# Kernel optimization log

Hardware: AMD Instinct MI355X
Metric: run time of the kernel (lower is better)

## Reference

```python
import jax, jax.numpy as jnp
import numpy as np

N, E, G, H, D = 30000, 480000, 128, 4, 64
NF, EF, GF, L = 92, 50, 108, 5
EPS = 1e-3  # keras BatchNormalization default epsilon


def _bn(t, g, b, m, v):
    # inference-mode batch norm with running stats
    return (t - m) * jax.lax.rsqrt(v + EPS) * g + b


def _forward(x, edge_attr, global_features,
             node_W, node_b, edge_W, edge_b,
             conv_W, conv_att, conv_bias, conv_bn_g, conv_bn_b, conv_bn_m, conv_bn_v,
             ga_W0, ga_b0, ga_bn0_g, ga_bn0_b, ga_bn0_m, ga_bn0_v,
             ga_W1, ga_b1, ga_bn1_g, ga_bn1_b, ga_bn1_m, ga_bn1_v,
             ga_W2, ga_b2, out_W0, out_b0, out_W1, out_b1,
             edge_index, batch_idx, num_graphs):
    lrelu = lambda t: jax.nn.leaky_relu(t, 0.2)
    row, col = edge_index[0], edge_index[1]
    n = x.shape[0]

    x = lrelu(x @ node_W + node_b)          # [N, D] node embedding
    ea = lrelu(edge_attr @ edge_W + edge_b)  # [E, D] edge embedding

    def conv(xc, p):
        W, att, bias, g, b, m, v = p
        xi = (jnp.concatenate([xc[row], ea], -1) @ W).reshape(-1, H, D)  # [E,H,D]
        xj = (jnp.concatenate([xc[col], ea], -1) @ W).reshape(-1, H, D)
        score = jnp.einsum('ehd,hd->eh', jnp.concatenate([xi, xj], -1), att)
        a = jnp.exp(_bn(lrelu(score), g, b, m, v))            # [E,H]
        norm = jax.ops.segment_sum(a, row, num_segments=n)    # edge softmax denom
        a = a / norm[row]
        msg = xj * a[..., None]                               # [E,H,D]
        # faithful to original: transpose then flat reshape before scatter-add
        msg = jnp.transpose(msg, (1, 0, 2)).reshape(-1, H * D)
        agg = jax.ops.segment_sum(msg, row, num_segments=n)
        out = agg.reshape(n, H, D).mean(axis=1) + bias
        return xc + out, None  # residual connection (done in GATGNN.call)

    x, _ = jax.lax.scan(conv, x, (conv_W, conv_att, conv_bias,
                                  conv_bn_g, conv_bn_b, conv_bn_m, conv_bn_v))

    # global attention pooling
    feat = jnp.concatenate([x, global_features[batch_idx]], -1)  # [N, D+GF]
    h = jax.nn.relu(_bn(feat @ ga_W0 + ga_b0, ga_bn0_g, ga_bn0_b, ga_bn0_m, ga_bn0_v))
    h = jax.nn.relu(_bn(h @ ga_W1 + ga_b1, ga_bn1_g, ga_bn1_b, ga_bn1_m, ga_bn1_v))
    a = jnp.exp(h @ ga_W2 + ga_b2)                               # [N,1]
    norm = jax.ops.segment_sum(a, batch_idx, num_segments=num_graphs)
    a = a / norm[batch_idx]
    pooled = jax.ops.segment_sum(x * a, batch_idx, num_segments=num_graphs)  # [G,D]
    out = jax.nn.relu(pooled @ out_W0 + out_b0) @ out_W1 + out_b1
    return out.squeeze(-1)  # output_dim == 1


def setup_inputs() -> dict:
    key = jax.random.key(0)
    ks = jax.random.split(key, 16)
    s = 0.05
    return {
        'x': jax.random.normal(ks[0], (N, NF), jnp.float32),
        'edge_attr': jax.random.normal(ks[1], (E, EF), jnp.float32),
        'global_features': jax.random.normal(ks[2], (G, GF), jnp.float32),
        'node_W': jax.random.normal(ks[3], (NF, D)) * s, 'node_b': jnp.zeros((D,)),
        'edge_W': jax.random.normal(ks[4], (EF, D)) * s, 'edge_b': jnp.zeros((D,)),
        'conv_W': jax.random.normal(ks[5], (L, 2 * D, H * D)) * s,
        'conv_att': jax.random.normal(ks[6], (L, H, 2 * D)) * s,
        'conv_bias': jnp.zeros((L, D)),
        'conv_bn_g': jnp.ones((L, H)), 'conv_bn_b': jnp.zeros((L, H)),
        'conv_bn_m': jnp.zeros((L, H)), 'conv_bn_v': jnp.ones((L, H)),
        'ga_W0': jax.random.normal(ks[7], (D + GF, D)) * s, 'ga_b0': jnp.zeros((D,)),
        'ga_bn0_g': jnp.ones((D,)), 'ga_bn0_b': jnp.zeros((D,)),
        'ga_bn0_m': jnp.zeros((D,)), 'ga_bn0_v': jnp.ones((D,)),
        'ga_W1': jax.random.normal(ks[8], (D, D)) * s, 'ga_b1': jnp.zeros((D,)),
        'ga_bn1_g': jnp.ones((D,)), 'ga_bn1_b': jnp.zeros((D,)),
        'ga_bn1_m': jnp.zeros((D,)), 'ga_bn1_v': jnp.ones((D,)),
        'ga_W2': jax.random.normal(ks[9], (D, 1)) * s, 'ga_b2': jnp.zeros((1,)),
        'out_W0': jax.random.normal(ks[10], (D, D)) * s, 'out_b0': jnp.zeros((D,)),
        'out_W1': jax.random.normal(ks[11], (D, 1)) * s, 'out_b1': jnp.zeros((1,)),
        'edge_index': jax.random.randint(ks[12], (2, E), 0, N),
        'batch_idx': jnp.sort(jax.random.randint(ks[13], (N,), 0, G)),
        'num_graphs': G,
    }


def reference(x, edge_attr, global_features, node_W, node_b, edge_W, edge_b,
              conv_W, conv_att, conv_bias, conv_bn_g, conv_bn_b, conv_bn_m, conv_bn_v,
              ga_W0, ga_b0, ga_bn0_g, ga_bn0_b, ga_bn0_m, ga_bn0_v,
              ga_W1, ga_b1, ga_bn1_g, ga_bn1_b, ga_bn1_m, ga_bn1_v,
              ga_W2, ga_b2, out_W0, out_b0, out_W1, out_b1,
              edge_index, batch_idx, num_graphs):
    return _forward(x, edge_attr, global_features, node_W, node_b, edge_W, edge_b,
                    conv_W, conv_att, conv_bias, conv_bn_g, conv_bn_b, conv_bn_m, conv_bn_v,
                    ga_W0, ga_b0, ga_bn0_g, ga_bn0_b, ga_bn0_m, ga_bn0_v,
                    ga_W1, ga_b1, ga_bn1_g, ga_bn1_b, ga_bn1_m, ga_bn1_v,
                    ga_W2, ga_b2, out_W0, out_b0, out_W1, out_b1,
                    edge_index, batch_idx, num_graphs)
```

## Files before the change

kernel.cpp:

```cpp
#include <hip/hip_runtime.h>

constexpr int N = 30000, E = 480000, G = 128, H = 4, D = 64;
constexpr int NF = 92, EF = 50, GF = 108, L = 5;
constexpr int EQ = E / 4;
constexpr float EPS = 1e-3f;

__device__ __forceinline__ float lrelu(float t) { return t > 0.f ? t : 0.2f * t; }

__device__ __forceinline__ unsigned short f2bf(float f) {
  unsigned int u = __float_as_uint(f);
  u += 0x7FFFu + ((u >> 16) & 1u);
  return (unsigned short)(u >> 16);
}
__device__ __forceinline__ float bf2f(unsigned short s) {
  return __uint_as_float(((unsigned int)s) << 16);
}

__global__ __launch_bounds__(256) void hist_kernel(const int* __restrict__ row,
                                                   int* __restrict__ deg) {
  int e = blockIdx.x * 256 + threadIdx.x;
  atomicAdd(&deg[row[e]], 1);
}

__global__ __launch_bounds__(1024) void scan_kernel(const int* __restrict__ deg,
                                                    int* __restrict__ start) {
  __shared__ int wsum[16];
  __shared__ int cbase;
  if (threadIdx.x == 0) cbase = 0;
  __syncthreads();
  int lane = threadIdx.x & 63, wave = threadIdx.x >> 6;
  for (int base = 0; base < N; base += 1024) {
    int i = base + (int)threadIdx.x;
    int v = (i < N) ? deg[i] : 0;
    int s = v;
#pragma unroll
    for (int off = 1; off < 64; off <<= 1) { int t = __shfl_up(s, off); if (lane >= off) s += t; }
    if (lane == 63) wsum[wave] = s;
    __syncthreads();
    if (wave == 0 && lane < 16) {
      int w = wsum[lane];
#pragma unroll
      for (int off = 1; off < 16; off <<= 1) { int t = __shfl_up(w, off); if (lane >= off) w += t; }
      wsum[lane] = w;
    }
    __syncthreads();
    int wbase = wave ? wsum[wave - 1] : 0;
    if (i < N) start[i] = cbase + wbase + (s - v);
    __syncthreads();
    if (threadIdx.x == 0) cbase += wsum[15];
    __syncthreads();
  }
  if (threadIdx.x == 0) start[N] = cbase;
}

__global__ __launch_bounds__(256) void fill_kernel(
    const int* __restrict__ row, const int* __restrict__ start, int* __restrict__ cur,
    int* __restrict__ eid_s) {
  int e = blockIdx.x * 256 + threadIdx.x;
  int r = row[e];
  int pos = start[r] + atomicAdd(&cur[r], 1);
  eid_s[pos] = e;
}

template <int K, bool BF16OUT>
__global__ __launch_bounds__(256) void embed6_kernel(
    const float* __restrict__ in, const float* __restrict__ W,
    const float* __restrict__ bias, float* __restrict__ outF,
    unsigned short* __restrict__ outB, int ntiles) {
  constexpr int KP = (K + 3) & ~3;
  __shared__ float xs[16][KP];
  int tid = threadIdx.x;
  int lane = tid & 63, wave = tid >> 6;
  for (int f = tid; f < 16 * KP; f += 256) xs[f / KP][f % KP] = 0.f;
  float wreg[KP];
#pragma unroll
  for (int k = 0; k < K; k++) wreg[k] = W[k * 64 + lane];
#pragma unroll
  for (int k = K; k < KP; k++) wreg[k] = 0.f;
  float bb = bias[lane];
  for (int t = blockIdx.x; t < ntiles; t += gridDim.x) {
    __syncthreads();
    for (int f = tid; f < 16 * K; f += 256) xs[f / K][f % K] = in[(size_t)t * 16 * K + f];
    __syncthreads();
    float a0 = 0.f, a1 = 0.f, a2 = 0.f, a3 = 0.f;
#pragma unroll
    for (int kc = 0; kc < KP / 4; kc++) {
      float4 x0 = *(const float4*)&xs[wave * 4 + 0][kc * 4];
      float4 x1 = *(const float4*)&xs[wave * 4 + 1][kc * 4];
      float4 x2 = *(const float4*)&xs[wave * 4 + 2][kc * 4];
      float4 x3 = *(const float4*)&xs[wave * 4 + 3][kc * 4];
      float w0 = wreg[kc * 4], w1 = wreg[kc * 4 + 1], w2 = wreg[kc * 4 + 2], w3 = wreg[kc * 4 + 3];
      a0 = fmaf(x0.x, w0, fmaf(x0.y, w1, fmaf(x0.z, w2, fmaf(x0.w, w3, a0))));
      a1 = fmaf(x1.x, w0, fmaf(x1.y, w1, fmaf(x1.z, w2, fmaf(x1.w, w3, a1))));
      a2 = fmaf(x2.x, w0, fmaf(x2.y, w1, fmaf(x2.z, w2, fmaf(x2.w, w3, a2))));
      a3 = fmaf(x3.x, w0, fmaf(x3.y, w1, fmaf(x3.z, w2, fmaf(x3.w, w3, a3))));
    }
    size_t o = ((size_t)t * 16 + wave * 4) * 64 + lane;
    float r0 = lrelu(a0 + bb), r1 = lrelu(a1 + bb), r2 = lrelu(a2 + bb), r3 = lrelu(a3 + bb);
    if (BF16OUT) {
      outB[o] = f2bf(r0); outB[o + 64] = f2bf(r1);
      outB[o + 128] = f2bf(r2); outB[o + 192] = f2bf(r3);
    } else {
      outF[o] = r0; outF[o + 64] = r1; outF[o + 128] = r2; outF[o + 192] = r3;
    }
  }
}

__global__ __launch_bounds__(256) void aes_watt_all_kernel(
    const float* __restrict__ conv_W, const float* __restrict__ conv_att,
    float* __restrict__ AesT, float* __restrict__ WattT) {
  int l = blockIdx.x;
  const float* W = conv_W + (size_t)l * 128 * 256;
  const float* att = conv_att + (size_t)l * H * 128;
  int t = threadIdx.x;
  {
    int h = t >> 6, k = t & 63;
    float acc = 0.f;
    for (int d = 0; d < 64; d++)
      acc = fmaf(W[(64 + k) * 256 + h * 64 + d], att[h * 128 + d] + att[h * 128 + 64 + d], acc);
    AesT[l * 256 + h * 64 + k] = acc;
  }
  for (int idx = t; idx < 512; idx += 256) {
    int hh = idx >> 6, k = idx & 63;
    int h = hh >> 1, ij = hh & 1;
    float acc = 0.f;
    for (int d = 0; d < 64; d++)
      acc = fmaf(W[k * 256 + h * 64 + d], att[h * 128 + ij * 64 + d], acc);
    WattT[l * 512 + idx] = acc;
  }
}

__global__ __launch_bounds__(256) void qs_kernel(
    const unsigned short* __restrict__ ea, const float* __restrict__ AesT,
    float* __restrict__ qsAll) {
  int tid = threadIdx.x;
  int e = blockIdx.x * 16 + (tid >> 4);
  int k4 = tid & 15;
  uint2 raw = *(const uint2*)&ea[(size_t)e * 64 + k4 * 4];
  float e0 = __uint_as_float(raw.x << 16);
  float e1 = __uint_as_float(raw.x & 0xFFFF0000u);
  float e2 = __uint_as_float(raw.y << 16);
  float e3 = __uint_as_float(raw.y & 0xFFFF0000u);
#pragma unroll
  for (int l = 0; l < L; l++) {
    float q0, q1, q2, q3;
    {
      float4 c0 = *(const float4*)&AesT[l * 256 + 0 * 64 + k4 * 4];
      float4 c1 = *(const float4*)&AesT[l * 256 + 1 * 64 + k4 * 4];
      float4 c2 = *(const float4*)&AesT[l * 256 + 2 * 64 + k4 * 4];
      float4 c3 = *(const float4*)&AesT[l * 256 + 3 * 64 + k4 * 4];
      q0 = e0 * c0.x + e1 * c0.y + e2 * c0.z + e3 * c0.w;
      q1 = e0 * c1.x + e1 * c1.y + e2 * c1.z + e3 * c1.w;
      q2 = e0 * c2.x + e1 * c2.y + e2 * c2.z + e3 * c2.w;
      q3 = e0 * c3.x + e1 * c3.y + e2 * c3.z + e3 * c3.w;
    }
#pragma unroll
    for (int off = 1; off < 16; off <<= 1) {
      q0 += __shfl_xor(q0, off); q1 += __shfl_xor(q1, off);
      q2 += __shfl_xor(q2, off); q3 += __shfl_xor(q3, off);
    }
    if (k4 < 4) {
      float qv = (k4 == 0) ? q0 : (k4 == 1) ? q1 : (k4 == 2) ? q2 : q3;
      qsAll[(size_t)l * E * 4 + (size_t)e * 4 + k4] = qv;
    }
  }
}

__global__ __launch_bounds__(256) void xw_kernel(
    const float* __restrict__ xc, const float* __restrict__ W, const float* __restrict__ WattT,
    unsigned short* __restrict__ xWh, float* __restrict__ pi, float* __restrict__ pj) {
  __shared__ float xs[16][64];
  __shared__ float wlT[8][68];
  int tid = threadIdx.x, blk = blockIdx.x, n0 = blk * 16;
  for (int f = tid; f < 1024; f += 256) xs[f >> 6][f & 63] = xc[(size_t)n0 * 64 + f];
  for (int f = tid; f < 512; f += 256) wlT[f >> 6][f & 63] = WattT[f];
  __syncthreads();
  float acc[16];
#pragma unroll
  for (int n = 0; n < 16; n++) acc[n] = 0.f;
#pragma unroll 4
  for (int kc = 0; kc < 16; kc++) {
    float w0 = W[(4 * kc + 0) * 256 + tid];
    float w1 = W[(4 * kc + 1) * 256 + tid];
    float w2 = W[(4 * kc + 2) * 256 + tid];
    float w3 = W[(4 * kc + 3) * 256 + tid];
#pragma unroll
    for (int n = 0; n < 16; n++) {
      float4 xv = *(const float4*)&xs[n][4 * kc];
      acc[n] = fmaf(xv.x, w0, fmaf(xv.y, w1, fmaf(xv.z, w2, fmaf(xv.w, w3, acc[n]))));
    }
  }
  int h = tid >> 6, dd = tid & 63;
#pragma unroll
  for (int n = 0; n < 16; n++)
    xWh[((size_t)h * N + (n0 + n)) * 64 + dd] = f2bf(acc[n]);
  if (tid < 128) {
    int n = tid >> 3, hh = tid & 7;
    float a = 0.f;
#pragma unroll
    for (int kc = 0; kc < 16; kc++) {
      float4 xv = *(const float4*)&xs[n][4 * kc];
      float4 wv = *(const float4*)&wlT[hh][4 * kc];
      a = fmaf(xv.x, wv.x, fmaf(xv.y, wv.y, fmaf(xv.z, wv.z, fmaf(xv.w, wv.w, a))));
    }
    int hq = hh >> 1, ij = hh & 1;
    float* dst = ij ? pj : pi;
    dst[(n0 + n) * 4 + hq] = a;
  }
}

__global__ __launch_bounds__(256) void score2_kernel(
    const float* __restrict__ qs, const float* __restrict__ pi, const float* __restrict__ pj,
    const int* __restrict__ row, const int* __restrict__ col,
    const float* __restrict__ bng, const float* __restrict__ bnb,
    const float* __restrict__ bnm, const float* __restrict__ bnv,
    float* __restrict__ aArr) {
  int e = blockIdx.x * 256 + threadIdx.x;
  int r = row[e], c = col[e];
  float4 q = ((const float4*)qs)[e];
  float4 piv = ((const float4*)pi)[r];
  float4 pjv = ((const float4*)pj)[c];
  float A0 = bng[0] * rsqrtf(bnv[0] + EPS), B0 = bnb[0] - bnm[0] * A0;
  float A1 = bng[1] * rsqrtf(bnv[1] + EPS), B1 = bnb[1] - bnm[1] * A1;
  float A2 = bng[2] * rsqrtf(bnv[2] + EPS), B2 = bnb[2] - bnm[2] * A2;
  float A3 = bng[3] * rsqrtf(bnv[3] + EPS), B3 = bnb[3] - bnm[3] * A3;
  float4 out;
  out.x = expf(lrelu(piv.x + pjv.x + q.x) * A0 + B0);
  out.y = expf(lrelu(piv.y + pjv.y + q.y) * A1 + B1);
  out.z = expf(lrelu(piv.z + pjv.z + q.z) * A2 + B2);
  out.w = expf(lrelu(piv.w + pjv.w + q.w) * A3 + B3);
  ((float4*)aArr)[e] = out;
}

__global__ __launch_bounds__(256) void normsum_kernel(
    const float* __restrict__ aArr, const int* __restrict__ start,
    const int* __restrict__ eid_s, float* __restrict__ inv) {
  int n = blockIdx.x * 256 + threadIdx.x;
  if (n >= N) return;
  int s0 = start[n], s1 = start[n + 1];
  float4 s = {0.f, 0.f, 0.f, 0.f};
  int p = s0;
  for (; p + 4 <= s1; p += 4) {
    int e0 = eid_s[p], e1 = eid_s[p + 1], e2 = eid_s[p + 2], e3 = eid_s[p + 3];
    float4 a0 = ((const float4*)aArr)[e0];
    float4 a1 = ((const float4*)aArr)[e1];
    float4 a2 = ((const float4*)aArr)[e2];
    float4 a3 = ((const float4*)aArr)[e3];
    s.x += (a0.x + a1.x) + (a2.x + a3.x);
    s.y += (a0.y + a1.y) + (a2.y + a3.y);
    s.z += (a0.z + a1.z) + (a2.z + a3.z);
    s.w += (a0.w + a1.w) + (a2.w + a3.w);
  }
  for (; p < s1; p++) {
    float4 a = ((const float4*)aArr)[eid_s[p]];
    s.x += a.x; s.y += a.y; s.z += a.z; s.w += a.w;
  }
  float4 iv;
  if (s1 > s0) { iv.x = 1.f / s.x; iv.y = 1.f / s.y; iv.z = 1.f / s.z; iv.w = 1.f / s.w; }
  else         { iv.x = iv.y = iv.z = iv.w = 0.f; }
  ((float4*)inv)[n] = iv;
}

__global__ __launch_bounds__(256) void div_kernel(
    const float* __restrict__ aArr, const float* __restrict__ inv,
    const int* __restrict__ row, float* __restrict__ aT) {
  int e = blockIdx.x * 256 + threadIdx.x;
  float4 a = ((const float4*)aArr)[e];
  float4 iv = ((const float4*)inv)[row[e]];
  aT[0 * E + e] = a.x * iv.x;
  aT[1 * E + e] = a.y * iv.y;
  aT[2 * E + e] = a.z * iv.z;
  aT[3 * E + e] = a.w * iv.w;
}

__global__ __launch_bounds__(256) void yquad_kernel(
    const float* __restrict__ aT, const unsigned short* __restrict__ ea,
    unsigned short* __restrict__ Ybf) {
  int q = blockIdx.x * 4 + (threadIdx.x >> 6);
  int lane = threadIdx.x & 63;
  const unsigned short* er = ea + (size_t)q * 256 + lane;
  float e0 = bf2f(er[0]), e1 = bf2f(er[64]), e2 = bf2f(er[128]), e3 = bf2f(er[192]);
#pragma unroll
  for (int h = 0; h < 4; h++) {
    float4 a = *(const float4*)&aT[(size_t)h * E + 4 * q];
    float y = fmaf(a.x, e0, fmaf(a.y, e1, fmaf(a.z, e2, a.w * e3)));
    Ybf[((size_t)h * EQ + q) * 64 + lane] = f2bf(y);
  }
}

__global__ __launch_bounds__(256) void scatter_kernel(
    const float* __restrict__ aT, const unsigned short* __restrict__ Ybf,
    const unsigned short* __restrict__ xWh,
    const int* __restrict__ start, const int* __restrict__ eid_s, const int* __restrict__ col,
    float* __restrict__ out1, float* __restrict__ Bacc) {
  int wave = threadIdx.x >> 6, lane = threadIdx.x & 63;
  int n = blockIdx.x * 4 + wave;
  int s0 = __builtin_amdgcn_readfirstlane(start[n]);
  int s1 = __builtin_amdgcn_readfirstlane(start[n + 1]);
  float m0 = 0.f, m1 = 0.f, m2 = 0.f, m3 = 0.f;
  float b0 = 0.f, b1 = 0.f, b2 = 0.f, b3 = 0.f;
  int p = s0;
  for (; p + 2 <= s1; p += 2) {
    int r1 = eid_s[p], r2 = eid_s[p + 1];
    int h1 = r1 / EQ, h2 = r2 / EQ;
    int e1 = (r1 - h1 * EQ) * 4, e2 = (r2 - h2 * EQ) * 4;
    float4 A1 = *(const float4*)&aT[(size_t)h1 * E + e1];
    float4 A2 = *(const float4*)&aT[(size_t)h2 * E + e2];
    int4 C1 = *(const int4*)&col[e1];
    int4 C2 = *(const int4*)&col[e2];
    const unsigned short* xw1 = xWh + (size_t)h1 * N * 64 + lane;
    const unsigned short* xw2 = xWh + (size_t)h2 * N * 64 + lane;
    float g10 = bf2f(xw1[(size_t)C1.x * 64]), g11 = bf2f(xw1[(size_t)C1.y * 64]);
    float g12 = bf2f(xw1[(size_t)C1.z * 64]), g13 = bf2f(xw1[(size_t)C1.w * 64]);
    float g20 = bf2f(xw2[(size_t)C2.x * 64]), g21 = bf2f(xw2[(size_t)C2.y * 64]);
    float g22 = bf2f(xw2[(size_t)C2.z * 64]), g23 = bf2f(xw2[(size_t)C2.w * 64]);
    float s1v = bf2f(Ybf[(size_t)r1 * 64 + lane]);
    float s2v = bf2f(Ybf[(size_t)r2 * 64 + lane]);
    m0 = fmaf(A1.x, g10, m0); m1 = fmaf(A1.y, g11, m1);
    m2 = fmaf(A1.z, g12, m2); m3 = fmaf(A1.w, g13, m3);
    m0 = fmaf(A2.x, g20, m0); m1 = fmaf(A2.y, g21, m1);
    m2 = fmaf(A2.z, g22, m2); m3 = fmaf(A2.w, g23, m3);
    if (h1 == 0) b0 += s1v; else if (h1 == 1) b1 += s1v; else if (h1 == 2) b2 += s1v; else b3 += s1v;
    if (h2 == 0) b0 += s2v; else if (h2 == 1) b1 += s2v; else if (h2 == 2) b2 += s2v; else b3 += s2v;
  }
  for (; p < s1; p++) {
    int r = eid_s[p];
    int h = r / EQ;
    int e0 = (r - h * EQ) * 4;
    float4 a = *(const float4*)&aT[(size_t)h * E + e0];
    int4 c = *(const int4*)&col[e0];
    const unsigned short* xwh = xWh + (size_t)h * N * 64 + lane;
    m0 = fmaf(a.x, bf2f(xwh[(size_t)c.x * 64]), m0);
    m1 = fmaf(a.y, bf2f(xwh[(size_t)c.y * 64]), m1);
    m2 = fmaf(a.z, bf2f(xwh[(size_t)c.z * 64]), m2);
    m3 = fmaf(a.w, bf2f(xwh[(size_t)c.w * 64]), m3);
    float s = bf2f(Ybf[(size_t)r * 64 + lane]);
    if (h == 0) b0 += s; else if (h == 1) b1 += s; else if (h == 2) b2 += s; else b3 += s;
  }
  out1[(size_t)n * 64 + lane] = (m0 + m1) + (m2 + m3);
  float* Bn = Bacc + (size_t)n * 256 + lane;
  Bn[0] = b0; Bn[64] = b1; Bn[128] = b2; Bn[192] = b3;
}

__global__ __launch_bounds__(256) void finish_kernel(
    const float* __restrict__ out1, const float* __restrict__ Bacc,
    const float* __restrict__ W, const float* __restrict__ bias, float* __restrict__ xc) {
  __shared__ float Bl[16][256];
  int tid = threadIdx.x, blk = blockIdx.x;
  for (int f = tid; f < 4096; f += 256) Bl[f >> 8][f & 255] = Bacc[(size_t)blk * 4096 + f];
  __syncthreads();
  int lane = tid & 63, wave = tid >> 6;
  float a0 = 0.f, a1 = 0.f, a2 = 0.f, a3 = 0.f;
#pragma unroll
  for (int h = 0; h < 4; h++) {
#pragma unroll 4
    for (int kc = 0; kc < 16; kc++) {
      float w0 = W[(64 + 4 * kc + 0) * 256 + h * 64 + lane];
      float w1 = W[(64 + 4 * kc + 1) * 256 + h * 64 + lane];
      float w2 = W[(64 + 4 * kc + 2) * 256 + h * 64 + lane];
      float w3 = W[(64 + 4 * kc + 3) * 256 + h * 64 + lane];
      float4 b0v = *(const float4*)&Bl[wave * 4 + 0][h * 64 + 4 * kc];
      float4 b1v = *(const float4*)&Bl[wave * 4 + 1][h * 64 + 4 * kc];
      float4 b2v = *(const float4*)&Bl[wave * 4 + 2][h * 64 + 4 * kc];
      float4 b3v = *(const float4*)&Bl[wave * 4 + 3][h * 64 + 4 * kc];
      a0 = fmaf(b0v.x, w0, fmaf(b0v.y, w1, fmaf(b0v.z, w2, fmaf(b0v.w, w3, a0))));
      a1 = fmaf(b1v.x, w0, fmaf(b1v.y, w1, fmaf(b1v.z, w2, fmaf(b1v.w, w3, a1))));
      a2 = fmaf(b2v.x, w0, fmaf(b2v.y, w1, fmaf(b2v.z, w2, fmaf(b2v.w, w3, a2))));
      a3 = fmaf(b3v.x, w0, fmaf(b3v.y, w1, fmaf(b3v.z, w2, fmaf(b3v.w, w3, a3))));
    }
  }
  float bb = bias[lane];
  size_t i0 = (size_t)(blk * 16 + wave * 4) * 64 + lane;
  xc[i0]       += bb + 0.25f * (out1[i0] + a0);
  xc[i0 + 64]  += bb + 0.25f * (out1[i0 + 64] + a1);
  xc[i0 + 128] += bb + 0.25f * (out1[i0 + 128] + a2);
  xc[i0 + 192] += bb + 0.25f * (out1[i0 + 192] + a3);
}

__global__ __launch_bounds__(256) void gacontrib_kernel(
    const float* __restrict__ gfeat, const float* __restrict__ W0,
    const float* __restrict__ b0, float* __restrict__ gc) {
  __shared__ float gs[16][GF];
  int tid = threadIdx.x, blk = blockIdx.x;
  int lane = tid & 63, wave = tid >> 6;
  for (int f = tid; f < 16 * GF; f += 256) gs[f / GF][f % GF] = gfeat[(size_t)blk * 16 * GF + f];
  float wreg[GF];
#pragma unroll
  for (int k = 0; k < GF; k++) wreg[k] = W0[(64 + k) * 64 + lane];
  __syncthreads();
  float a0 = 0.f, a1 = 0.f, a2 = 0.f, a3 = 0.f;
#pragma unroll
  for (int kc = 0; kc < GF / 4; kc++) {
    float4 x0 = *(const float4*)&gs[wave * 4 + 0][kc * 4];
    float4 x1 = *(const float4*)&gs[wave * 4 + 1][kc * 4];
    float4 x2 = *(const float4*)&gs[wave * 4 + 2][kc * 4];
    float4 x3 = *(const float4*)&gs[wave * 4 + 3][kc * 4];
    float w0 = wreg[kc * 4], w1 = wreg[kc * 4 + 1], w2 = wreg[kc * 4 + 2], w3 = wreg[kc * 4 + 3];
    a0 = fmaf(x0.x, w0, fmaf(x0.y, w1, fmaf(x0.z, w2, fmaf(x0.w, w3, a0))));
    a1 = fmaf(x1.x, w0, fmaf(x1.y, w1, fmaf(x1.z, w2, fmaf(x1.w, w3, a1))));
    a2 = fmaf(x2.x, w0, fmaf(x2.y, w1, fmaf(x2.z, w2, fmaf(x2.w, w3, a2))));
    a3 = fmaf(x3.x, w0, fmaf(x3.y, w1, fmaf(x3.z, w2, fmaf(x3.w, w3, a3))));
  }
  float bb = b0[lane];
  size_t o = ((size_t)blk * 16 + wave * 4) * 64 + lane;
  gc[o]       = a0 + bb;
  gc[o + 64]  = a1 + bb;
  gc[o + 128] = a2 + bb;
  gc[o + 192] = a3 + bb;
}

__global__ __launch_bounds__(256) void ga0_kernel(
    const float* __restrict__ xc, const float* __restrict__ gc, const int* __restrict__ batch,
    const float* __restrict__ W0,
    const float* __restrict__ g0, const float* __restrict__ bb0,
    const float* __restrict__ m0, const float* __restrict__ v0,
    float* __restrict__ hout, int ntiles) {
  __shared__ float xs[16][64];
  __shared__ int bl[16];
  int tid = threadIdx.x, lane = tid & 63, wave = tid >> 6;
  float wreg[64];
#pragma unroll
  for (int k = 0; k < 64; k++) wreg[k] = W0[k * 64 + lane];
  float sc = rsqrtf(v0[lane] + EPS) * g0[lane];
  float mm = m0[lane], be = bb0[lane];
  for (int t = blockIdx.x; t < ntiles; t += gridDim.x) {
    __syncthreads();
    if (tid < 16) bl[tid] = batch[t * 16 + tid];
    for (int f = tid; f < 1024; f += 256) xs[f >> 6][f & 63] = xc[(size_t)t * 1024 + f];
    __syncthreads();
    float a0 = 0.f, a1 = 0.f, a2 = 0.f, a3 = 0.f;
#pragma unroll
    for (int kc = 0; kc < 16; kc++) {
      float4 x0 = *(const float4*)&xs[wave * 4 + 0][kc * 4];
      float4 x1 = *(const float4*)&xs[wave * 4 + 1][kc * 4];
      float4 x2 = *(const float4*)&xs[wave * 4 + 2][kc * 4];
      float4 x3 = *(const float4*)&xs[wave * 4 + 3][kc * 4];
      float w0 = wreg[kc * 4], w1 = wreg[kc * 4 + 1], w2 = wreg[kc * 4 + 2], w3 = wreg[kc * 4 + 3];
      a0 = fmaf(x0.x, w0, fmaf(x0.y, w1, fmaf(x0.z, w2, fmaf(x0.w, w3, a0))));
      a1 = fmaf(x1.x, w0, fmaf(x1.y, w1, fmaf(x1.z, w2, fmaf(x1.w, w3, a1))));
      a2 = fmaf(x2.x, w0, fmaf(x2.y, w1, fmaf(x2.z, w2, fmaf(x2.w, w3, a2))));
      a3 = fmaf(x3.x, w0, fmaf(x3.y, w1, fmaf(x3.z, w2, fmaf(x3.w, w3, a3))));
    }
    a0 += gc[(size_t)bl[wave * 4 + 0] * 64 + lane];
    a1 += gc[(size_t)bl[wave * 4 + 1] * 64 + lane];
    a2 += gc[(size_t)bl[wave * 4 + 2] * 64 + lane];
    a3 += gc[(size_t)bl[wave * 4 + 3] * 64 + lane];
    size_t o = ((size_t)t * 16 + wave * 4) * 64 + lane;
    hout[o]       = fmaxf((a0 - mm) * sc + be, 0.f);
    hout[o + 64]  = fmaxf((a1 - mm) * sc + be, 0.f);
    hout[o + 128] = fmaxf((a2 - mm) * sc + be, 0.f);
    hout[o + 192] = fmaxf((a3 - mm) * sc + be, 0.f);
  }
}

__global__ __launch_bounds__(256) void ga1_kernel(
    const float* __restrict__ hbuf, const int* __restrict__ batch,
    const float* __restrict__ W1, const float* __restrict__ b1,
    const float* __restrict__ g1, const float* __restrict__ bb1,
    const float* __restrict__ m1, const float* __restrict__ v1,
    const float* __restrict__ W2, const float* __restrict__ b2,
    float* __restrict__ a_un, float* __restrict__ norm_g, int ntiles) {
  __shared__ float hsh[16][64];
  __shared__ int bl[16];
  int tid = threadIdx.x, lane = tid & 63, wave = tid >> 6;
  float wreg[64];
#pragma unroll
  for (int k = 0; k < 64; k++) wreg[k] = W1[k * 64 + lane];
  float sc1 = rsqrtf(v1[lane] + EPS) * g1[lane];
  float mm1 = m1[lane], be1 = bb1[lane], bb1v = b1[lane];
  float w2v = W2[lane], b2v = b2[0];
  for (int t = blockIdx.x; t < ntiles; t += gridDim.x) {
    __syncthreads();
    if (tid < 16) bl[tid] = batch[t * 16 + tid];
    for (int f = tid; f < 1024; f += 256) hsh[f >> 6][f & 63] = hbuf[(size_t)t * 1024 + f];
    __syncthreads();
    float c0 = 0.f, c1 = 0.f, c2 = 0.f, c3 = 0.f;
#pragma unroll
    for (int kc = 0; kc < 16; kc++) {
      float4 x0 = *(const float4*)&hsh[wave * 4 + 0][kc * 4];
      float4 x1 = *(const float4*)&hsh[wave * 4 + 1][kc * 4];
      float4 x2 = *(const float4*)&hsh[wave * 4 + 2][kc * 4];
      float4 x3 = *(const float4*)&hsh[wave * 4 + 3][kc * 4];
      float w0 = wreg[kc * 4], w1 = wreg[kc * 4 + 1], w2 = wreg[kc * 4 + 2], w3 = wreg[kc * 4 + 3];
      c0 = fmaf(x0.x, w0, fmaf(x0.y, w1, fmaf(x0.z, w2, fmaf(x0.w, w3, c0))));
      c1 = fmaf(x1.x, w0, fmaf(x1.y, w1, fmaf(x1.z, w2, fmaf(x1.w, w3, c1))));
      c2 = fmaf(x2.x, w0, fmaf(x2.y, w1, fmaf(x2.z, w2, fmaf(x2.w, w3, c2))));
      c3 = fmaf(x3.x, w0, fmaf(x3.y, w1, fmaf(x3.z, w2, fmaf(x3.w, w3, c3))));
    }
    float p0 = fmaxf((c0 + bb1v - mm1) * sc1 + be1, 0.f) * w2v;
    float p1 = fmaxf((c1 + bb1v - mm1) * sc1 + be1, 0.f) * w2v;
    float p2 = fmaxf((c2 + bb1v - mm1) * sc1 + be1, 0.f) * w2v;
    float p3 = fmaxf((c3 + bb1v - mm1) * sc1 + be1, 0.f) * w2v;
#pragma unroll
    for (int off = 1; off < 64; off <<= 1) {
      p0 += __shfl_xor(p0, off); p1 += __shfl_xor(p1, off);
      p2 += __shfl_xor(p2, off); p3 += __shfl_xor(p3, off);
    }
    if (lane < 4) {
      float pv = (lane == 0) ? p0 : (lane == 1) ? p1 : (lane == 2) ? p2 : p3;
      float a = expf(pv + b2v);
      int node = t * 16 + wave * 4 + lane;
      a_un[node] = a;
      atomicAdd(&norm_g[bl[wave * 4 + lane]], a);
    }
  }
}

__global__ __launch_bounds__(256) void pool_kernel(
    const float* __restrict__ xc, const float* __restrict__ a_un,
    const float* __restrict__ norm_g, const int* __restrict__ batch,
    float* __restrict__ pooled) {
  int n = blockIdx.x * 4 + (threadIdx.x >> 6);
  int d = threadIdx.x & 63;
  int b = batch[n];
  float coef = a_un[n] / norm_g[b];
  atomicAdd(&pooled[b * 64 + d], xc[(size_t)n * 64 + d] * coef);
}

__global__ __launch_bounds__(256) void final_kernel(
    const float* __restrict__ pooled, const float* __restrict__ W0,
    const float* __restrict__ b0, const float* __restrict__ W1,
    const float* __restrict__ b1, float* __restrict__ out) {
  int g = blockIdx.x * 4 + (threadIdx.x >> 6);
  int d = threadIdx.x & 63;
  float pv = pooled[g * 64 + d];
  float acc = b0[d];
  for (int k = 0; k < 64; k++) acc = fmaf(__shfl(pv, k), W0[k * 64 + d], acc);
  acc = fmaxf(acc, 0.f);
  float p = acc * W1[d];
  for (int off = 1; off < 64; off <<= 1) p += __shfl_xor(p, off);
  if (d == 0) out[g] = p + b1[0];
}

extern "C" void kernel_launch(void* const* d_in, const int* in_sizes, int n_in,
                              void* d_out, int out_size, void* d_ws, size_t ws_size,
                              hipStream_t stream) {
  (void)in_sizes; (void)n_in; (void)out_size; (void)ws_size;
  const float* x_in    = (const float*)d_in[0];
  const float* ea_in   = (const float*)d_in[1];
  const float* gf      = (const float*)d_in[2];
  const float* node_W  = (const float*)d_in[3];
  const float* node_b  = (const float*)d_in[4];
  const float* edge_W  = (const float*)d_in[5];
  const float* edge_b  = (const float*)d_in[6];
  const float* conv_W  = (const float*)d_in[7];
  const float* conv_att= (const float*)d_in[8];
  const float* conv_bias=(const float*)d_in[9];
  const float* bn_g = (const float*)d_in[10];
  const float* bn_b = (const float*)d_in[11];
  const float* bn_m = (const float*)d_in[12];
  const float* bn_v = (const float*)d_in[13];
  const float* ga_W0 = (const float*)d_in[14]; const float* ga_b0 = (const float*)d_in[15];
  const float* ga0g = (const float*)d_in[16];  const float* ga0b = (const float*)d_in[17];
  const float* ga0m = (const float*)d_in[18];  const float* ga0v = (const float*)d_in[19];
  const float* ga_W1 = (const float*)d_in[20]; const float* ga_b1 = (const float*)d_in[21];
  const float* ga1g = (const float*)d_in[22];  const float* ga1b = (const float*)d_in[23];
  const float* ga1m = (const float*)d_in[24];  const float* ga1v = (const float*)d_in[25];
  const float* ga_W2 = (const float*)d_in[26]; const float* ga_b2 = (const float*)d_in[27];
  const float* out_W0 = (const float*)d_in[28]; const float* out_b0 = (const float*)d_in[29];
  const float* out_W1 = (const float*)d_in[30]; const float* out_b1 = (const float*)d_in[31];
  const int* eidx  = (const int*)d_in[32];
  const int* row   = eidx;
  const int* col   = eidx + E;
  const int* batch = (const int*)d_in[33];

  float* ws = (float*)d_ws;
  size_t off = 0;
  auto alloc = [&](size_t n) { float* p = ws + off; off += (n + 63) & ~(size_t)63; return p; };
  float* x_cur  = alloc((size_t)N * D);
  unsigned short* ea_bf = (unsigned short*)alloc((size_t)E * 32);
  unsigned short* xWh   = (unsigned short*)alloc((size_t)N * 128);
  unsigned short* Ybf   = (unsigned short*)alloc((size_t)E * 32);
  float* pi     = alloc((size_t)N * 4);
  float* pj     = alloc((size_t)N * 4);
  float* aArr   = alloc((size_t)E * 4);
  float* aT     = alloc((size_t)E * 4);
  float* invA   = alloc((size_t)N * 4);
  float* out1   = alloc((size_t)N * 64);
  float* Bacc   = alloc((size_t)N * 256);
  float* AesT   = alloc(L * 256);
  float* WattT  = alloc(L * 512);
  float* a_un   = alloc(N);
  float* norm_g = alloc(G);
  float* pooled = alloc((size_t)G * 64);
  int* start = (int*)alloc(N + 1);
  int* eid_s = (int*)alloc(E);
  float* qsAll  = alloc((size_t)L * E * 4);
  int* deg = (int*)xWh;
  int* cur = deg + N;
  float* gcontrib = (float*)xWh;
  float* hbuf     = Bacc;

  hipMemsetAsync(deg, 0, (size_t)2 * N * sizeof(int), stream);
  hist_kernel<<<E / 256, 256, 0, stream>>>(row, deg);
  scan_kernel<<<1, 1024, 0, stream>>>(deg, start);
  fill_kernel<<<E / 256, 256, 0, stream>>>(row, start, cur, eid_s);

  embed6_kernel<NF, false><<<960, 256, 0, stream>>>(x_in, node_W, node_b, x_cur, nullptr, N / 16);
  embed6_kernel<EF, true><<<1920, 256, 0, stream>>>(ea_in, edge_W, edge_b, nullptr, ea_bf, E / 16);

  aes_watt_all_kernel<<<L, 256, 0, stream>>>(conv_W, conv_att, AesT, WattT);
  qs_kernel<<<E / 16, 256, 0, stream>>>(ea_bf, AesT, qsAll);

  for (int l = 0; l < L; l++) {
    const float* W = conv_W + (size_t)l * 128 * 256;
    xw_kernel<<<N / 16, 256, 0, stream>>>(x_cur, W, WattT + l * 512, xWh, pi, pj);
    score2_kernel<<<E / 256, 256, 0, stream>>>(qsAll + (size_t)l * E * 4, pi, pj, row, col,
                                               bn_g + l * H, bn_b + l * H,
                                               bn_m + l * H, bn_v + l * H, aArr);
    normsum_kernel<<<(N + 255) / 256, 256, 0, stream>>>(aArr, start, eid_s, invA);
    div_kernel<<<E / 256, 256, 0, stream>>>(aArr, invA, row, aT);
    yquad_kernel<<<EQ / 4, 256, 0, stream>>>(aT, ea_bf, Ybf);
    scatter_kernel<<<N / 4, 256, 0, stream>>>(aT, Ybf, xWh, start, eid_s, col, out1, Bacc);
    finish_kernel<<<N / 16, 256, 0, stream>>>(out1, Bacc, W, conv_bias + l * D, x_cur);
  }

  hipMemsetAsync(norm_g, 0, G * sizeof(float), stream);
  hipMemsetAsync(pooled, 0, (size_t)G * 64 * sizeof(float), stream);
  gacontrib_kernel<<<G / 16, 256, 0, stream>>>(gf, ga_W0, ga_b0, gcontrib);
  ga0_kernel<<<960, 256, 0, stream>>>(x_cur, gcontrib, batch, ga_W0,
                                      ga0g, ga0b, ga0m, ga0v, hbuf, N / 16);
  ga1_kernel<<<960, 256, 0, stream>>>(hbuf, batch, ga_W1, ga_b1,
                                      ga1g, ga1b, ga1m, ga1v, ga_W2, ga_b2,
                                      a_un, norm_g, N / 16);
  pool_kernel<<<N / 4, 256, 0, stream>>>(x_cur, a_un, norm_g, batch, pooled);
  final_kernel<<<G / 4, 256, 0, stream>>>(pooled, out_W0, out_b0, out_W1, out_b1,
                                          (float*)d_out);
}
```

Baseline: 1.442 ms.

## Fuse softmax division into quad kernel, precompute per-quad gathered messages, double-buffer embed loads

The separate division kernel is removed. The quad kernel now normalizes attention inline and also gathers xWh by col to produce a bf16 per-quad message Z alongside Y. The scatter kernel then only streams Z and Y rows per sorted edge, so it no longer does random col/xWh gathers inside the per-node loop. The embedding kernels gain register-staged double buffering of input tiles to overlap global loads with compute. In exchange this adds a new E*32 bf16 buffer, extra write traffic, and one more bf16 rounding of the aggregated message.

```diff
diff --git a/kernel.cpp b/kernel.cpp
--- a/kernel.cpp
+++ b/kernel.cpp
@@ -63,32 +63,47 @@
 }
 
 template <int K, bool BF16OUT>
-__global__ __launch_bounds__(256) void embed6_kernel(
+__global__ __launch_bounds__(256) void embed7_kernel(
     const float* __restrict__ in, const float* __restrict__ W,
     const float* __restrict__ bias, float* __restrict__ outF,
     unsigned short* __restrict__ outB, int ntiles) {
   constexpr int KP = (K + 3) & ~3;
-  __shared__ float xs[16][KP];
-  int tid = threadIdx.x;
-  int lane = tid & 63, wave = tid >> 6;
-  for (int f = tid; f < 16 * KP; f += 256) xs[f / KP][f % KP] = 0.f;
+  constexpr int NL = (16 * K + 255) / 256;
+  __shared__ float xs[2][16][KP];
+  int tid = threadIdx.x, lane = tid & 63, wave = tid >> 6;
+  if (K != KP) {
+    for (int f = tid; f < 2 * 16 * KP; f += 256)
+      if (f % KP >= K) ((float*)xs)[f] = 0.f;
+  }
   float wreg[KP];
 #pragma unroll
   for (int k = 0; k < K; k++) wreg[k] = W[k * 64 + lane];
 #pragma unroll
   for (int k = K; k < KP; k++) wreg[k] = 0.f;
   float bb = bias[lane];
-  for (int t = blockIdx.x; t < ntiles; t += gridDim.x) {
-    __syncthreads();
-    for (int f = tid; f < 16 * K; f += 256) xs[f / K][f % K] = in[(size_t)t * 16 * K + f];
-    __syncthreads();
+  float stage[NL];
+  int t = blockIdx.x;
+  if (t < ntiles) {
+#pragma unroll
+    for (int i = 0; i < NL; i++) { int f = tid + i * 256; if (f < 16 * K) stage[i] = in[(size_t)t * 16 * K + f]; }
+#pragma unroll
+    for (int i = 0; i < NL; i++) { int f = tid + i * 256; if (f < 16 * K) xs[0][f / K][f % K] = stage[i]; }
+  }
+  __syncthreads();
+  int cur = 0;
+  for (; t < ntiles; t += gridDim.x) {
+    int nxt = t + gridDim.x;
+    if (nxt < ntiles) {
+#pragma unroll
+      for (int i = 0; i < NL; i++) { int f = tid + i * 256; if (f < 16 * K) stage[i] = in[(size_t)nxt * 16 * K + f]; }
+    }
     float a0 = 0.f, a1 = 0.f, a2 = 0.f, a3 = 0.f;
 #pragma unroll
     for (int kc = 0; kc < KP / 4; kc++) {
-      float4 x0 = *(const float4*)&xs[wave * 4 + 0][kc * 4];
-      float4 x1 = *(const float4*)&xs[wave * 4 + 1][kc * 4];
-      float4 x2 = *(const float4*)&xs[wave * 4 + 2][kc * 4];
-      float4 x3 = *(const float4*)&xs[wave * 4 + 3][kc * 4];
+      float4 x0 = *(const float4*)&xs[cur][wave * 4 + 0][kc * 4];
+      float4 x1 = *(const float4*)&xs[cur][wave * 4 + 1][kc * 4];
+      float4 x2 = *(const float4*)&xs[cur][wave * 4 + 2][kc * 4];
+      float4 x3 = *(const float4*)&xs[cur][wave * 4 + 3][kc * 4];
       float w0 = wreg[kc * 4], w1 = wreg[kc * 4 + 1], w2 = wreg[kc * 4 + 2], w3 = wreg[kc * 4 + 3];
       a0 = fmaf(x0.x, w0, fmaf(x0.y, w1, fmaf(x0.z, w2, fmaf(x0.w, w3, a0))));
       a1 = fmaf(x1.x, w0, fmaf(x1.y, w1, fmaf(x1.z, w2, fmaf(x1.w, w3, a1))));
@@ -103,6 +118,12 @@
     } else {
       outF[o] = r0; outF[o + 64] = r1; outF[o + 128] = r2; outF[o + 192] = r3;
     }
+    if (nxt < ntiles) {
+#pragma unroll
+      for (int i = 0; i < NL; i++) { int f = tid + i * 256; if (f < 16 * K) xs[cur ^ 1][f / K][f % K] = stage[i]; }
+    }
+    __syncthreads();
+    cur ^= 1;
   }
 }
 
@@ -261,83 +282,81 @@
   ((float4*)inv)[n] = iv;
 }
 
-__global__ __launch_bounds__(256) void div_kernel(
-    const float* __restrict__ aArr, const float* __restrict__ inv,
-    const int* __restrict__ row, float* __restrict__ aT) {
-  int e = blockIdx.x * 256 + threadIdx.x;
-  float4 a = ((const float4*)aArr)[e];
-  float4 iv = ((const float4*)inv)[row[e]];
-  aT[0 * E + e] = a.x * iv.x;
-  aT[1 * E + e] = a.y * iv.y;
-  aT[2 * E + e] = a.z * iv.z;
-  aT[3 * E + e] = a.w * iv.w;
-}
-
-__global__ __launch_bounds__(256) void yquad_kernel(
-    const float* __restrict__ aT, const unsigned short* __restrict__ ea,
-    unsigned short* __restrict__ Ybf) {
+__global__ __launch_bounds__(256) void zyquad_kernel(
+    const float* __restrict__ aArr, const float* __restrict__ invA,
+    const unsigned short* __restrict__ ea, const unsigned short* __restrict__ xWh,
+    const int* __restrict__ row, const int* __restrict__ col,
+    unsigned short* __restrict__ Ybf, unsigned short* __restrict__ Zbf) {
   int q = blockIdx.x * 4 + (threadIdx.x >> 6);
   int lane = threadIdx.x & 63;
   const unsigned short* er = ea + (size_t)q * 256 + lane;
   float e0 = bf2f(er[0]), e1 = bf2f(er[64]), e2 = bf2f(er[128]), e3 = bf2f(er[192]);
+  int4 rw = *(const int4*)&row[4 * q];
+  int4 cl = *(const int4*)&col[4 * q];
+  float4 A0 = ((const float4*)aArr)[4 * q + 0];
+  float4 A1 = ((const float4*)aArr)[4 * q + 1];
+  float4 A2 = ((const float4*)aArr)[4 * q + 2];
+  float4 A3 = ((const float4*)aArr)[4 * q + 3];
+  float4 I0 = ((const float4*)invA)[rw.x];
+  float4 I1 = ((const float4*)invA)[rw.y];
+  float4 I2 = ((const float4*)invA)[rw.z];
+  float4 I3 = ((const float4*)invA)[rw.w];
+  float c0[4] = {A0.x * I0.x, A0.y * I0.y, A0.z * I0.z, A0.w * I0.w};
+  float c1[4] = {A1.x * I1.x, A1.y * I1.y, A1.z * I1.z, A1.w * I1.w};
+  float c2[4] = {A2.x * I2.x, A2.y * I2.y, A2.z * I2.z, A2.w * I2.w};
+  float c3[4] = {A3.x * I3.x, A3.y * I3.y, A3.z * I3.z, A3.w * I3.w};
 #pragma unroll
   for (int h = 0; h < 4; h++) {
-    float4 a = *(const float4*)&aT[(size_t)h * E + 4 * q];
-    float y = fmaf(a.x, e0, fmaf(a.y, e1, fmaf(a.z, e2, a.w * e3)));
-    Ybf[((size_t)h * EQ + q) * 64 + lane] = f2bf(y);
-  }
-}
-
-__global__ __launch_bounds__(256) void scatter_kernel(
-    const float* __restrict__ aT, const unsigned short* __restrict__ Ybf,
-    const unsigned short* __restrict__ xWh,
-    const int* __restrict__ start, const int* __restrict__ eid_s, const int* __restrict__ col,
+    const unsigned short* xw = xWh + (size_t)h * N * 64 + lane;
+    float g0 = bf2f(xw[(size_t)cl.x * 64]);
+    float g1 = bf2f(xw[(size_t)cl.y * 64]);
+    float g2 = bf2f(xw[(size_t)cl.z * 64]);
+    float g3 = bf2f(xw[(size_t)cl.w * 64]);
+    float y = fmaf(c0[h], e0, fmaf(c1[h], e1, fmaf(c2[h], e2, c3[h] * e3)));
+    float z = fmaf(c0[h], g0, fmaf(c1[h], g1, fmaf(c2[h], g2, c3[h] * g3)));
+    size_t r = (size_t)h * EQ + q;
+    Ybf[r * 64 + lane] = f2bf(y);
+    Zbf[r * 64 + lane] = f2bf(z);
+  }
+}
+
+__global__ __launch_bounds__(256) void scatter2_kernel(
+    const unsigned short* __restrict__ Zbf, const unsigned short* __restrict__ Ybf,
+    const int* __restrict__ start, const int* __restrict__ eid_s,
     float* __restrict__ out1, float* __restrict__ Bacc) {
   int wave = threadIdx.x >> 6, lane = threadIdx.x & 63;
   int n = blockIdx.x * 4 + wave;
   int s0 = __builtin_amdgcn_readfirstlane(start[n]);
   int s1 = __builtin_amdgcn_readfirstlane(start[n + 1]);
-  float m0 = 0.f, m1 = 0.f, m2 = 0.f, m3 = 0.f;
+  float m = 0.f;
   float b0 = 0.f, b1 = 0.f, b2 = 0.f, b3 = 0.f;
   int p = s0;
-  for (; p + 2 <= s1; p += 2) {
-    int r1 = eid_s[p], r2 = eid_s[p + 1];
-    int h1 = r1 / EQ, h2 = r2 / EQ;
-    int e1 = (r1 - h1 * EQ) * 4, e2 = (r2 - h2 * EQ) * 4;
-    float4 A1 = *(const float4*)&aT[(size_t)h1 * E + e1];
-    float4 A2 = *(const float4*)&aT[(size_t)h2 * E + e2];
-    int4 C1 = *(const int4*)&col[e1];
-    int4 C2 = *(const int4*)&col[e2];
-    const unsigned short* xw1 = xWh + (size_t)h1 * N * 64 + lane;
-    const unsigned short* xw2 = xWh + (size_t)h2 * N * 64 + lane;
-    float g10 = bf2f(xw1[(size_t)C1.x * 64]), g11 = bf2f(xw1[(size_t)C1.y * 64]);
-    float g12 = bf2f(xw1[(size_t)C1.z * 64]), g13 = bf2f(xw1[(size_t)C1.w * 64]);
-    float g20 = bf2f(xw2[(size_t)C2.x * 64]), g21 = bf2f(xw2[(size_t)C2.y * 64]);
-    float g22 = bf2f(xw2[(size_t)C2.z * 64]), g23 = bf2f(xw2[(size_t)C2.w * 64]);
-    float s1v = bf2f(Ybf[(size_t)r1 * 64 + lane]);
-    float s2v = bf2f(Ybf[(size_t)r2 * 64 + lane]);
-    m0 = fmaf(A1.x, g10, m0); m1 = fmaf(A1.y, g11, m1);
-    m2 = fmaf(A1.z, g12, m2); m3 = fmaf(A1.w, g13, m3);
-    m0 = fmaf(A2.x, g20, m0); m1 = fmaf(A2.y, g21, m1);
-    m2 = fmaf(A2.z, g22, m2); m3 = fmaf(A2.w, g23, m3);
-    if (h1 == 0) b0 += s1v; else if (h1 == 1) b1 += s1v; else if (h1 == 2) b2 += s1v; else b3 += s1v;
-    if (h2 == 0) b0 += s2v; else if (h2 == 1) b1 += s2v; else if (h2 == 2) b2 += s2v; else b3 += s2v;
+  for (; p + 4 <= s1; p += 4) {
+    int r0 = eid_s[p], r1 = eid_s[p + 1], r2 = eid_s[p + 2], r3 = eid_s[p + 3];
+    float z0 = bf2f(Zbf[(size_t)r0 * 64 + lane]);
+    float z1 = bf2f(Zbf[(size_t)r1 * 64 + lane]);
+    float z2 = bf2f(Zbf[(size_t)r2 * 64 + lane]);
+    float z3 = bf2f(Zbf[(size_t)r3 * 64 + lane]);
+    float y0 = bf2f(Ybf[(size_t)r0 * 64 + lane]);
+    float y1 = bf2f(Ybf[(size_t)r1 * 64 + lane]);
+    float y2 = bf2f(Ybf[(size_t)r2 * 64 + lane]);
+    float y3 = bf2f(Ybf[(size_t)r3 * 64 + lane]);
+    m += (z0 + z1) + (z2 + z3);
+    int h0 = r0 / EQ, h1 = r1 / EQ, h2 = r2 / EQ, h3 = r3 / EQ;
+    if (h0 == 0) b0 += y0; else if (h0 == 1) b1 += y0; else if (h0 == 2) b2 += y0; else b3 += y0;
+    if (h1 == 0) b0 += y1; else if (h1 == 1) b1 += y1; else if (h1 == 2) b2 += y1; else b3 += y1;
+    if (h2 == 0) b0 += y2; else if (h2 == 1) b1 += y2; else if (h2 == 2) b2 += y2; else b3 += y2;
+    if (h3 == 0) b0 += y3; else if (h3 == 1) b1 += y3; else if (h3 == 2) b2 += y3; else b3 += y3;
   }
   for (; p < s1; p++) {
     int r = eid_s[p];
+    float z = bf2f(Zbf[(size_t)r * 64 + lane]);
+    float y = bf2f(Ybf[(size_t)r * 64 + lane]);
+    m += z;
     int h = r / EQ;
-    int e0 = (r - h * EQ) * 4;
-    float4 a = *(const float4*)&aT[(size_t)h * E + e0];
-    int4 c = *(const int4*)&col[e0];
-    const unsigned short* xwh = xWh + (size_t)h * N * 64 + lane;
-    m0 = fmaf(a.x, bf2f(xwh[(size_t)c.x * 64]), m0);
-    m1 = fmaf(a.y, bf2f(xwh[(size_t)c.y * 64]), m1);
-    m2 = fmaf(a.z, bf2f(xwh[(size_t)c.z * 64]), m2);
-    m3 = fmaf(a.w, bf2f(xwh[(size_t)c.w * 64]), m3);
-    float s = bf2f(Ybf[(size_t)r * 64 + lane]);
-    if (h == 0) b0 += s; else if (h == 1) b1 += s; else if (h == 2) b2 += s; else b3 += s;
-  }
-  out1[(size_t)n * 64 + lane] = (m0 + m1) + (m2 + m3);
+    if (h == 0) b0 += y; else if (h == 1) b1 += y; else if (h == 2) b2 += y; else b3 += y;
+  }
+  out1[(size_t)n * 64 + lane] = m;
   float* Bn = Bacc + (size_t)n * 256 + lane;
   Bn[0] = b0; Bn[64] = b1; Bn[128] = b2; Bn[192] = b3;
 }
@@ -571,10 +590,10 @@
   unsigned short* ea_bf = (unsigned short*)alloc((size_t)E * 32);
   unsigned short* xWh   = (unsigned short*)alloc((size_t)N * 128);
   unsigned short* Ybf   = (unsigned short*)alloc((size_t)E * 32);
+  unsigned short* Zbf   = (unsigned short*)alloc((size_t)E * 32);
   float* pi     = alloc((size_t)N * 4);
   float* pj     = alloc((size_t)N * 4);
   float* aArr   = alloc((size_t)E * 4);
-  float* aT     = alloc((size_t)E * 4);
   float* invA   = alloc((size_t)N * 4);
   float* out1   = alloc((size_t)N * 64);
   float* Bacc   = alloc((size_t)N * 256);
@@ -596,8 +615,8 @@
   scan_kernel<<<1, 1024, 0, stream>>>(deg, start);
   fill_kernel<<<E / 256, 256, 0, stream>>>(row, start, cur, eid_s);
 
-  embed6_kernel<NF, false><<<960, 256, 0, stream>>>(x_in, node_W, node_b, x_cur, nullptr, N / 16);
-  embed6_kernel<EF, true><<<1920, 256, 0, stream>>>(ea_in, edge_W, edge_b, nullptr, ea_bf, E / 16);
+  embed7_kernel<NF, false><<<960, 256, 0, stream>>>(x_in, node_W, node_b, x_cur, nullptr, N / 16);
+  embed7_kernel<EF, true><<<1920, 256, 0, stream>>>(ea_in, edge_W, edge_b, nullptr, ea_bf, E / 16);
 
   aes_watt_all_kernel<<<L, 256, 0, stream>>>(conv_W, conv_att, AesT, WattT);
   qs_kernel<<<E / 16, 256, 0, stream>>>(ea_bf, AesT, qsAll);
@@ -609,9 +628,8 @@
                                                bn_g + l * H, bn_b + l * H,
                                                bn_m + l * H, bn_v + l * H, aArr);
     normsum_kernel<<<(N + 255) / 256, 256, 0, stream>>>(aArr, start, eid_s, invA);
-    div_kernel<<<E / 256, 256, 0, stream>>>(aArr, invA, row, aT);
-    yquad_kernel<<<EQ / 4, 256, 0, stream>>>(aT, ea_bf, Ybf);
-    scatter_kernel<<<N / 4, 256, 0, stream>>>(aT, Ybf, xWh, start, eid_s, col, out1, Bacc);
+    zyquad_kernel<<<EQ / 4, 256, 0, stream>>>(aArr, invA, ea_bf, xWh, row, col, Ybf, Zbf);
+    scatter2_kernel<<<N / 4, 256, 0, stream>>>(Zbf, Ybf, start, eid_s, out1, Bacc);
     finish_kernel<<<N / 16, 256, 0, stream>>>(out1, Bacc, W, conv_bias + l * D, x_cur);
   }
 
```

Result: faster. 1.383 ms (-4.1%).
